# Performance work log

Measured on AMD Instinct MI355X. Metric: run time of the kernel, lower is better.

The kernel has to match this reference:

```python
import jax, jax.numpy as jnp
import numpy as np

N, D = 8192, 128

def _rbf_kernel(x, y):
    # InfoVAE-style kernel: exp(-mean((x_i - y_j)^2) / dim) = exp(-sqdist / dim^2)
    dim = x.shape[1]
    x2 = jnp.sum(x * x, axis=1)              # [n]
    y2 = jnp.sum(y * y, axis=1)              # [m]
    sqdist = x2[:, None] + y2[None, :] - 2.0 * (x @ y.T)  # [n, m]
    return jnp.exp(-sqdist / (dim * dim))


def setup_inputs() -> dict:
    key = jax.random.key(0)
    k1, k2 = jax.random.split(key)
    inputs = jax.random.normal(k1, (N, D), dtype=jnp.float32)
    true_samples = jax.random.normal(k2, (N, D), dtype=jnp.float32)
    return {"inputs": inputs, "true_samples": true_samples}


def reference(inputs, true_samples):
    x = true_samples  # samples from standard normal prior
    y = inputs
    k_xx = _rbf_kernel(x, x)
    k_yy = _rbf_kernel(y, y)
    k_xy = _rbf_kernel(x, y)
    mmd = jnp.mean(k_xx) + jnp.mean(k_yy) - 2.0 * jnp.mean(k_xy)
    return mmd
```

## Files before the change

kernel.cpp:

```cpp
#include <hip/hip_runtime.h>
#include <hip/hip_bf16.h>
#include <math.h>


#define NN 8192
#define DD 128
#define TZ 16384
#define SPLIT 12
#define NBLK (64 * SPLIT)

typedef __attribute__((ext_vector_type(8))) short bf16x8;
typedef __attribute__((ext_vector_type(4))) float f32x4;
typedef __attribute__((ext_vector_type(2))) float f32x2;

#if __has_builtin(__builtin_amdgcn_exp2f)
#define EXP2F __builtin_amdgcn_exp2f
#else
#define EXP2F exp2f
#endif

constexpr float LOG2E = 0x1.715476p+0f;
constexpr float S2 = LOG2E / 8192.0f;

constexpr size_t PLANE = 1048576;

#define LDS_RED 32768

constexpr size_t WS_NORM = 2048;
constexpr size_t WS_Z    = WS_NORM + (size_t)TZ * sizeof(float);

__device__ __forceinline__ void gload_lds16(const void* g, void* l) {
  __builtin_amdgcn_global_load_lds(
      (const __attribute__((address_space(1))) void*)g,
      (__attribute__((address_space(3))) void*)l, 16, 0, 0);
}

__global__ __launch_bounds__(256) void prep(
    const float* __restrict__ X, const float* __restrict__ Y,
    char* __restrict__ Zs, float* __restrict__ normZ,
    double* __restrict__ sums) {
  if (blockIdx.x == 0) sums[threadIdx.x] = 0.0;

  const int row = blockIdx.x * 4 + (threadIdx.x >> 6);
  const int lane = threadIdx.x & 63;
  const float* __restrict__ src =
      (row < NN) ? (X + (size_t)row * DD) : (Y + (size_t)(row - NN) * DD);
  const float2 v = *reinterpret_cast<const float2*>(src + 2 * lane);

  float n = v.x * v.x + v.y * v.y;

  const int ks = lane >> 4;
  const int quadc = (lane >> 2) & 3;
  const int inner = (lane & 3) * 4;
  char* dst = Zs + (size_t)ks * PLANE + (size_t)row * 64 +
              ((quadc ^ ((row >> 1) & 3)) << 4) + inner;
  *reinterpret_cast<__hip_bfloat162*>(dst) =
      __hip_bfloat162{__float2bfloat16(v.x), __float2bfloat16(v.y)};

#pragma unroll
  for (int o = 32; o > 0; o >>= 1) n += __shfl_down(n, o);
  if (lane == 0) normZ[row] = n * (-LOG2E / 16384.0f);
}

__global__ __launch_bounds__(256, 3) void mmd_mfma(
    const char* __restrict__ Zs, const float* __restrict__ normZ,
    double* __restrict__ sums) {
  __shared__ alignas(16) char lds[LDS_RED + 64];

  const int bid = blockIdx.x;
  const int p = bid / SPLIT, s = bid % SPLIT;
  const int q = 127 - p;
  const int n1 = (127 - p - s) / SPLIT + 1;
  const int u0 = s + SPLIT * n1 - (128 - p);
  const int n2 = (u0 <= p) ? (p - u0) / SPLIT + 1 : 0;

  const int segI[2]  = {p, q};
  const int segJ0[2] = {p + s, q + u0};
  const int segN[2]  = {n1, n2};

  const int tid = threadIdx.x;
  const int lane = tid & 63, wave = tid >> 6;
  const int wr = wave >> 1, wc = wave & 1;
  const int lr = lane & 15, quad = lane >> 4;

  const int csw = (quad ^ ((lr >> 1) & 3)) << 4;
  const char* aRd = lds + (wr * 64 + lr) * 64 + csw;
  const size_t bOff = (size_t)(wc * 64 + lr) * 64 + csw;

  bf16x8 a[4], b0[4], b1[4];
  f32x4 ar[4];

#define LOADA(ks) do {                                                      \
    _Pragma("unroll")                                                       \
    for (int i = 0; i < 4; ++i)                                             \
      a[i] = *reinterpret_cast<const bf16x8*>(aRd + (ks) * 8192 + i * 1024);\
  } while (0)

#define LOADB(dst, base, pl) do {                                           \
    _Pragma("unroll")                                                       \
    for (int j = 0; j < 4; ++j)                                             \
      dst[j] = *reinterpret_cast<const bf16x8*>(                            \
          (base) + (size_t)(pl) * PLANE + j * 1024);                        \
  } while (0)

#define MFMAS(bb) do {                                                      \
    __builtin_amdgcn_s_setprio(1);                                          \
    _Pragma("unroll")                                                       \
    for (int i = 0; i < 4; ++i)                                             \
      _Pragma("unroll")                                                     \
      for (int j = 0; j < 4; ++j)                                           \
        acc[i][j] = __builtin_amdgcn_mfma_f32_16x16x32_bf16(                \
            a[i], bb[j], acc[i][j], 0, 0, 0);                               \
    __builtin_amdgcn_s_setprio(0);                                          \
  } while (0)

  const f32x2 s2v = {S2, S2};
  double blockAcc = 0.0;

  for (int seg = 0; seg < 2; ++seg) {
    const int I = segI[seg];
    const int nIter = segN[seg];
    if (nIter == 0) continue;
    int J = segJ0[seg];

    const float* nzA = normZ + I * 128 + wr * 64;
#pragma unroll
    for (int i = 0; i < 4; ++i)
      ar[i] = *reinterpret_cast<const f32x4*>(nzA + i * 16 + quad * 4);

    const char* srcA0 = Zs + (size_t)(I * 128 + wave * 32) * 64 + lane * 16;
    char* ldwA = lds + wave * 2048;
#pragma unroll
    for (int ks = 0; ks < 4; ++ks) {
      gload_lds16(srcA0 + (size_t)ks * PLANE,        ldwA + ks * 8192);
      gload_lds16(srcA0 + (size_t)ks * PLANE + 1024, ldwA + ks * 8192 + 1024);
    }

    const char* bbase = Zs + (size_t)J * 8192 + bOff;
    LOADB(b0, bbase, 0);
    asm volatile("s_waitcnt vmcnt(0)\n\ts_barrier" ::: "memory");

    for (int it = 0; it < nIter; ++it) {
      const char* bnext = (it + 1 < nIter) ? bbase + SPLIT * 8192 : bbase;
      f32x4 acc[4][4] = {};

      LOADB(b1, bbase, 1);
      LOADA(0);
      __builtin_amdgcn_sched_barrier(0);
      MFMAS(b0);

      LOADB(b0, bbase, 2);
      LOADA(1);
      __builtin_amdgcn_sched_barrier(0);
      MFMAS(b1);

      LOADB(b1, bbase, 3);
      LOADA(2);
      __builtin_amdgcn_sched_barrier(0);
      MFMAS(b0);

      LOADB(b0, bnext, 0);
      LOADA(3);
      __builtin_amdgcn_sched_barrier(0);
      MFMAS(b1);

      const float* nzB = normZ + J * 128 + wc * 64;
      float cb[4];
#pragma unroll
      for (int j = 0; j < 4; ++j) cb[j] = nzB[j * 16 + lr];

      f32x2 part01 = {0.f, 0.f}, part23 = {0.f, 0.f};
#pragma unroll
      for (int i = 0; i < 4; ++i) {
        const f32x2 ar01 = {ar[i].x, ar[i].y};
        const f32x2 ar23 = {ar[i].z, ar[i].w};
#pragma unroll
        for (int j = 0; j < 4; ++j) {
          const f32x2 rb2 = {cb[j], cb[j]};
          const f32x2 base01 = ar01 + rb2;
          const f32x2 base23 = ar23 + rb2;
          const f32x2 acc01 = {acc[i][j][0], acc[i][j][1]};
          const f32x2 acc23 = {acc[i][j][2], acc[i][j][3]};
          const f32x2 arg01 = __builtin_elementwise_fma(acc01, s2v, base01);
          const f32x2 arg23 = __builtin_elementwise_fma(acc23, s2v, base23);
          part01 += (f32x2){EXP2F(arg01.x), EXP2F(arg01.y)};
          part23 += (f32x2){EXP2F(arg23.x), EXP2F(arg23.y)};
        }
      }
      const f32x2 ps = part01 + part23;
      double w = ((I < 64) == (J < 64)) ? 1.0 : -1.0;
      if (I != J) w += w;
      blockAcc += (double)(ps.x + ps.y) * w;

      J += SPLIT;
      bbase = bnext;
    }

    __syncthreads();
  }

#undef LOADA
#undef LOADB
#undef MFMAS

#pragma unroll
  for (int o = 32; o > 0; o >>= 1) blockAcc += __shfl_down(blockAcc, o);
  double* red = reinterpret_cast<double*>(lds + LDS_RED);
  if (lane == 0) red[wave] = blockAcc;
  __syncthreads();
  if (tid == 0)
    atomicAdd(&sums[bid & 255], red[0] + red[1] + red[2] + red[3]);
}

__global__ void finish(const double* __restrict__ s, float* __restrict__ out) {
  double v = s[threadIdx.x] + s[threadIdx.x + 64] + s[threadIdx.x + 128] +
             s[threadIdx.x + 192];
#pragma unroll
  for (int o = 32; o > 0; o >>= 1) v += __shfl_down(v, o);
  if (threadIdx.x == 0)
    out[0] = (float)(v * (1.0 / ((double)NN * (double)NN)));
}

extern "C" void kernel_launch(void* const* d_in, const int* in_sizes, int n_in,
                              void* d_out, int out_size, void* d_ws, size_t ws_size,
                              hipStream_t stream) {
  const float* y_inputs = (const float*)d_in[0];
  const float* x_true   = (const float*)d_in[1];
  float* out = (float*)d_out;

  char* ws = (char*)d_ws;
  double* sums = (double*)ws;
  float* normZ = (float*)(ws + WS_NORM);
  char* Zs = ws + WS_Z;

  prep<<<TZ / 4, 256, 0, stream>>>(x_true, y_inputs, Zs, normZ, sums);
  mmd_mfma<<<NBLK, 256, 0, stream>>>(Zs, normZ, sums);
  finish<<<1, 64, 0, stream>>>(sums, out);
}
```

Measured before the change: 101.9 us.

## Raise occupancy, single-buffer B fragments, and fuse final reduction into MFMA kernel

Raises SPLIT from 12 to 16 so more blocks are launched, and raises the launch-bounds occupancy hint from 3 to 4. To make room in registers it drops the double-buffered B fragments and instead loads the next B plane after each MFMA group, and it reloads the row norms inside the loop rather than keeping them live. It also removes the separate finish kernel: the last block, found through an atomic counter, performs the final reduction. The cost is less latency hiding for the B loads and extra global loads of the norms per iteration, in exchange for higher occupancy and one fewer launch.

```diff
diff --git a/kernel.cpp b/kernel.cpp
--- a/kernel.cpp
+++ b/kernel.cpp
@@ -6,7 +6,7 @@
 #define NN 8192
 #define DD 128
 #define TZ 16384
-#define SPLIT 12
+#define SPLIT 16
 #define NBLK (64 * SPLIT)
 
 typedef __attribute__((ext_vector_type(8))) short bf16x8;
@@ -26,7 +26,8 @@
 
 #define LDS_RED 32768
 
-constexpr size_t WS_NORM = 2048;
+constexpr size_t WS_CTR  = 2048;
+constexpr size_t WS_NORM = 2560;
 constexpr size_t WS_Z    = WS_NORM + (size_t)TZ * sizeof(float);
 
 __device__ __forceinline__ void gload_lds16(const void* g, void* l) {
@@ -38,8 +39,11 @@
 __global__ __launch_bounds__(256) void prep(
     const float* __restrict__ X, const float* __restrict__ Y,
     char* __restrict__ Zs, float* __restrict__ normZ,
-    double* __restrict__ sums) {
-  if (blockIdx.x == 0) sums[threadIdx.x] = 0.0;
+    double* __restrict__ sums, unsigned* __restrict__ ctr) {
+  if (blockIdx.x == 0) {
+    sums[threadIdx.x] = 0.0;
+    if (threadIdx.x == 0) *ctr = 0u;
+  }
 
   const int row = blockIdx.x * 4 + (threadIdx.x >> 6);
   const int lane = threadIdx.x & 63;
@@ -62,9 +66,10 @@
   if (lane == 0) normZ[row] = n * (-LOG2E / 16384.0f);
 }
 
-__global__ __launch_bounds__(256, 3) void mmd_mfma(
+__global__ __launch_bounds__(256, 4) void mmd_mfma(
     const char* __restrict__ Zs, const float* __restrict__ normZ,
-    double* __restrict__ sums) {
+    double* __restrict__ sums, unsigned* __restrict__ ctr,
+    float* __restrict__ out) {
   __shared__ alignas(16) char lds[LDS_RED + 64];
 
   const int bid = blockIdx.x;
@@ -87,8 +92,7 @@
   const char* aRd = lds + (wr * 64 + lr) * 64 + csw;
   const size_t bOff = (size_t)(wc * 64 + lr) * 64 + csw;
 
-  bf16x8 a[4], b0[4], b1[4];
-  f32x4 ar[4];
+  bf16x8 a[4], b[4];
 
 #define LOADA(ks) do {                                                      \
     _Pragma("unroll")                                                       \
@@ -96,22 +100,20 @@
       a[i] = *reinterpret_cast<const bf16x8*>(aRd + (ks) * 8192 + i * 1024);\
   } while (0)
 
-#define LOADB(dst, base, pl) do {                                           \
+#define LOADB(base, pl) do {                                                \
     _Pragma("unroll")                                                       \
     for (int j = 0; j < 4; ++j)                                             \
-      dst[j] = *reinterpret_cast<const bf16x8*>(                            \
+      b[j] = *reinterpret_cast<const bf16x8*>(                              \
           (base) + (size_t)(pl) * PLANE + j * 1024);                        \
   } while (0)
 
-#define MFMAS(bb) do {                                                      \
-    __builtin_amdgcn_s_setprio(1);                                          \
+#define MFMAS() do {                                                        \
     _Pragma("unroll")                                                       \
     for (int i = 0; i < 4; ++i)                                             \
       _Pragma("unroll")                                                     \
       for (int j = 0; j < 4; ++j)                                           \
         acc[i][j] = __builtin_amdgcn_mfma_f32_16x16x32_bf16(                \
-            a[i], bb[j], acc[i][j], 0, 0, 0);                               \
-    __builtin_amdgcn_s_setprio(0);                                          \
+            a[i], b[j], acc[i][j], 0, 0, 0);                                \
   } while (0)
 
   const f32x2 s2v = {S2, S2};
@@ -123,11 +125,6 @@
     if (nIter == 0) continue;
     int J = segJ0[seg];
 
-    const float* nzA = normZ + I * 128 + wr * 64;
-#pragma unroll
-    for (int i = 0; i < 4; ++i)
-      ar[i] = *reinterpret_cast<const f32x4*>(nzA + i * 16 + quad * 4);
-
     const char* srcA0 = Zs + (size_t)(I * 128 + wave * 32) * 64 + lane * 16;
     char* ldwA = lds + wave * 2048;
 #pragma unroll
@@ -137,33 +134,43 @@
     }
 
     const char* bbase = Zs + (size_t)J * 8192 + bOff;
-    LOADB(b0, bbase, 0);
+    LOADB(bbase, 0);
     asm volatile("s_waitcnt vmcnt(0)\n\ts_barrier" ::: "memory");
+
+    const float* nzA = normZ + I * 128 + wr * 64;
 
     for (int it = 0; it < nIter; ++it) {
       const char* bnext = (it + 1 < nIter) ? bbase + SPLIT * 8192 : bbase;
       f32x4 acc[4][4] = {};
 
-      LOADB(b1, bbase, 1);
       LOADA(0);
       __builtin_amdgcn_sched_barrier(0);
-      MFMAS(b0);
-
-      LOADB(b0, bbase, 2);
+      MFMAS();
+      __builtin_amdgcn_sched_barrier(0);
+      LOADB(bbase, 1);
+
       LOADA(1);
       __builtin_amdgcn_sched_barrier(0);
-      MFMAS(b1);
-
-      LOADB(b1, bbase, 3);
+      MFMAS();
+      __builtin_amdgcn_sched_barrier(0);
+      LOADB(bbase, 2);
+
       LOADA(2);
       __builtin_amdgcn_sched_barrier(0);
-      MFMAS(b0);
-
-      LOADB(b0, bnext, 0);
+      MFMAS();
+      __builtin_amdgcn_sched_barrier(0);
+      LOADB(bbase, 3);
+
       LOADA(3);
       __builtin_amdgcn_sched_barrier(0);
-      MFMAS(b1);
-
+      MFMAS();
+      __builtin_amdgcn_sched_barrier(0);
+      LOADB(bnext, 0);
+
+      f32x4 ar[4];
+#pragma unroll
+      for (int i = 0; i < 4; ++i)
+        ar[i] = *reinterpret_cast<const f32x4*>(nzA + i * 16 + quad * 4);
       const float* nzB = normZ + J * 128 + wc * 64;
       float cb[4];
 #pragma unroll
@@ -203,22 +210,28 @@
 #undef LOADB
 #undef MFMAS
 
+  __shared__ double red[4];
+  __shared__ int lastFlag;
 #pragma unroll
   for (int o = 32; o > 0; o >>= 1) blockAcc += __shfl_down(blockAcc, o);
-  double* red = reinterpret_cast<double*>(lds + LDS_RED);
   if (lane == 0) red[wave] = blockAcc;
   __syncthreads();
-  if (tid == 0)
+  if (tid == 0) {
     atomicAdd(&sums[bid & 255], red[0] + red[1] + red[2] + red[3]);
-}
-
-__global__ void finish(const double* __restrict__ s, float* __restrict__ out) {
-  double v = s[threadIdx.x] + s[threadIdx.x + 64] + s[threadIdx.x + 128] +
-             s[threadIdx.x + 192];
-#pragma unroll
-  for (int o = 32; o > 0; o >>= 1) v += __shfl_down(v, o);
-  if (threadIdx.x == 0)
-    out[0] = (float)(v * (1.0 / ((double)NN * (double)NN)));
+    __threadfence();
+    lastFlag = (atomicAdd(ctr, 1u) == NBLK - 1);
+  }
+  __syncthreads();
+  if (wave == 0 && lastFlag) {
+    double v = 0.0;
+#pragma unroll
+    for (int k = 0; k < 4; ++k)
+      v += atomicAdd(&sums[lane * 4 + k], 0.0);
+#pragma unroll
+    for (int o = 32; o > 0; o >>= 1) v += __shfl_down(v, o);
+    if (lane == 0)
+      out[0] = (float)(v * (1.0 / ((double)NN * (double)NN)));
+  }
 }
 
 extern "C" void kernel_launch(void* const* d_in, const int* in_sizes, int n_in,
@@ -230,10 +243,10 @@
 
   char* ws = (char*)d_ws;
   double* sums = (double*)ws;
+  unsigned* ctr = (unsigned*)(ws + WS_CTR);
   float* normZ = (float*)(ws + WS_NORM);
   char* Zs = ws + WS_Z;
 
-  prep<<<TZ / 4, 256, 0, stream>>>(x_true, y_inputs, Zs, normZ, sums);
-  mmd_mfma<<<NBLK, 256, 0, stream>>>(Zs, normZ, sums);
-  finish<<<1, 64, 0, stream>>>(sums, out);
-}
+  prep<<<TZ / 4, 256, 0, stream>>>(x_true, y_inputs, Zs, normZ, sums, ctr);
+  mmd_mfma<<<NBLK, 256, 0, stream>>>(Zs, normZ, sums, ctr, out);
+}
```

After: 121.4 us. 19.2% more time.
